# Kernel optimization log

Hardware: AMD Instinct MI355X
Metric: run time of the kernel (lower is better)

## Reference

```python
import jax, jax.numpy as jnp
import numpy as np

EPS = 1e-8  # torch CosineSimilarity default eps


def setup_inputs() -> dict:
    key = jax.random.key(0)
    k1, k2, k3, k4 = jax.random.split(key, 4)
    cur_insts = jax.random.randint(k1, (200, 1024), 0, 50000)          # [S, B] token ids
    W = jax.random.normal(k2, (50000, 300), dtype=jnp.float32)          # embedding table
    train_embs = jax.random.normal(k3, (100000, 300), dtype=jnp.float32)  # pooled train embeddings
    y_train = jax.random.randint(k4, (100000,), 0, 1000)                # train labels
    return {"cur_insts": cur_insts, "W": W, "train_embs": train_embs, "y_train": y_train}


def reference(cur_insts, W, train_embs, y_train):
    # Embed + mean-pool over the sequence axis (dim 0 in the torch code)
    x = W[cur_insts].mean(axis=0)                                   # [B, d]
    # Cosine similarity: x.y / (max(||x||,eps) * max(||y||,eps))
    xn = jnp.maximum(jnp.linalg.norm(x, axis=1, keepdims=True), EPS)        # [B, 1]
    tn = jnp.maximum(jnp.linalg.norm(train_embs, axis=1, keepdims=True), EPS)  # [N, 1]
    sims = (x @ train_embs.T) / (xn * tn.T)                         # [B, N]
    nn_idx = jnp.argmax(sims, axis=1)                               # [B]
    scores = jnp.max(sims, axis=1)                                  # [B]
    y_pred = y_train[nn_idx]                                        # [B]
    return y_pred, scores
```

## Files before the change

### kernel.cpp

```cpp
#include <hip/hip_runtime.h>
#include <hip/hip_bf16.h>
#include <stdint.h>

#define EPS 1e-8f

typedef __attribute__((ext_vector_type(8))) short bf16x8;
typedef __attribute__((ext_vector_type(4))) float f32x4;
typedef unsigned long long u64;
typedef unsigned int u32;

constexpr int SEQ = 200;
constexpr int B_  = 1024;
constexpr int D_  = 300;
constexpr int DP  = 320;
constexpr int NT  = 100000;
constexpr int BM = 256, BN = 128, BK = 64;
constexpr int NSTRIP = 784;
constexpr int NTP = NSTRIP * BN;
constexpr int POOL_BLOCKS = B_;
constexpr int TN2_BLOCKS = NTP / 8;
constexpr int CAND_MAX = 8192;
constexpr int RESCORE_BLOCKS = 2048;
#define MARGIN 2e-3f

__device__ __forceinline__ unsigned short f2bf(float f) {
    u32 b = __float_as_uint(f);
    return (unsigned short)((b + 0x7fffu + ((b >> 16) & 1u)) >> 16);
}
__device__ __forceinline__ u32 simkey(float s) {
    u32 b = __float_as_uint(s);
    return (b & 0x80000000u) ? ~b : (b | 0x80000000u);
}
__device__ __forceinline__ void gload_lds16(const void* g, void* l) {
    __builtin_amdgcn_global_load_lds(
        (const __attribute__((address_space(1))) unsigned int*)g,
        (__attribute__((address_space(3))) unsigned int*)l, 16, 0, 0);
}

__global__ __launch_bounds__(640) void pool_kernel(
    const int* __restrict__ ids, const float* __restrict__ W,
    float* __restrict__ x, unsigned short* __restrict__ xh,
    float* __restrict__ rxn, u32* __restrict__ count)
{
    const int tid = threadIdx.x;
    const int w = tid >> 6, lane = tid & 63;
    const int b = blockIdx.x;
    if (b == 0 && tid == 0) *count = 0;
    __shared__ int sid[SEQ];
    __shared__ float part[10 * 304];
    __shared__ float red[320];
    __shared__ float rns_s;
    for (int s = tid; s < SEQ; s += 640) sid[s] = ids[s * B_ + b];
    __syncthreads();
    float4 a0 = make_float4(0.f, 0.f, 0.f, 0.f);
    float4 a1 = make_float4(0.f, 0.f, 0.f, 0.f);
    for (int s = w; s < SEQ; s += 10) {
        const float4* Wr = (const float4*)(W + (size_t)sid[s] * D_);
        float4 v = Wr[lane];
        a0.x += v.x; a0.y += v.y; a0.z += v.z; a0.w += v.w;
        if (lane < 11) {
            float4 u = Wr[64 + lane];
            a1.x += u.x; a1.y += u.y; a1.z += u.z; a1.w += u.w;
        }
    }
    *(float4*)&part[w * 304 + lane * 4] = a0;
    if (lane < 11) *(float4*)&part[w * 304 + 256 + lane * 4] = a1;
    else if (lane == 11) {
        float4 z = make_float4(0.f, 0.f, 0.f, 0.f);
        *(float4*)&part[w * 304 + 256 + lane * 4] = z;
    }
    __syncthreads();
    float xv = 0.f;
    if (tid < 304) {
        float s = 0.f;
        #pragma unroll
        for (int ww = 0; ww < 10; ++ww) s += part[ww * 304 + tid];
        xv = s * (1.0f / SEQ);
    }
    if (tid < 320) red[tid] = (tid < D_) ? xv * xv : 0.f;
    __syncthreads();
    if (tid < 64) {
        float s = 0.f;
        #pragma unroll
        for (int i = 0; i < 5; ++i) s += red[tid + i * 64];
        #pragma unroll
        for (int m = 32; m >= 1; m >>= 1) s += __shfl_xor(s, m, 64);
        if (tid == 0) {
            float r = 1.0f / fmaxf(sqrtf(s), EPS);
            rxn[b] = r;
            rns_s = r;
        }
    }
    __syncthreads();
    const float rns = rns_s;
    if (tid < 320) {
        if (tid < D_) {
            x[(size_t)b * D_ + tid] = xv;
            xh[(size_t)b * DP + tid] = f2bf(xv * rns);
        } else {
            xh[(size_t)b * DP + tid] = 0;
        }
    }
}

__global__ __launch_bounds__(512) void tnorm_kernel(
    const float* __restrict__ T, unsigned short* __restrict__ Tb)
{
    const int tid = threadIdx.x;
    const int w = tid >> 6, lane = tid & 63;
    const int n = blockIdx.x * 8 + w;
    if (n >= NTP) return;
    ushort4* tb = (ushort4*)(Tb + (size_t)n * DP);
    if (n >= NT) {
        ushort4 z = {0, 0, 0, 0};
        tb[lane] = z;
        if (lane < 16) tb[64 + lane] = z;
        return;
    }
    const float4* Tr = (const float4*)(T + (size_t)n * D_);
    float4 v = Tr[lane];
    float s = v.x * v.x + v.y * v.y + v.z * v.z + v.w * v.w;
    float4 w2 = make_float4(0.f, 0.f, 0.f, 0.f);
    if (lane < 11) {
        w2 = Tr[64 + lane];
        s += w2.x * w2.x + w2.y * w2.y + w2.z * w2.z + w2.w * w2.w;
    }
    #pragma unroll
    for (int m = 32; m >= 1; m >>= 1) s += __shfl_xor(s, m, 64);
    const float rns = 1.0f / fmaxf(sqrtf(s), EPS);
    ushort4 o;
    o.x = f2bf(v.x * rns); o.y = f2bf(v.y * rns);
    o.z = f2bf(v.z * rns); o.w = f2bf(v.w * rns);
    tb[lane] = o;
    if (lane < 16) {
        ushort4 p = {0, 0, 0, 0};
        if (lane < 11) {
            p.x = f2bf(w2.x * rns); p.y = f2bf(w2.y * rns);
            p.z = f2bf(w2.z * rns); p.w = f2bf(w2.w * rns);
        }
        tb[64 + lane] = p;
    }
}

__global__ __launch_bounds__(512, 2) void gemm_hh_kernel(
    const unsigned short* __restrict__ Ah, const unsigned short* __restrict__ Tb,
    float* __restrict__ blockmax)
{
    __shared__ unsigned short sA[BM * BK];
    __shared__ unsigned short sB[BN * BK];
    __shared__ float sBestF[BM * 2];

    const int tid = threadIdx.x;
    const int g = blockIdx.x;
    const int k8 = g & 7;
    const int h = g >> 3;
    const int bMi = h & 3;
    const int strip = ((h >> 2) << 3) | k8;

    const int lane = tid & 63, wid = tid >> 6;
    const int wm = wid >> 1, wn = wid & 1;
    const int quad = lane >> 4, l15 = lane & 15;

    const unsigned short* pA[4];
    int laA[4];
    #pragma unroll
    for (int j = 0; j < 4; ++j) {
        int L = (j * 8 + wid) * 64 + lane;
        int r = L >> 3, c = (L & 7) ^ (r & 7);
        laA[j] = (j * 8 + wid) * 1024;
        pA[j] = Ah + (size_t)(bMi * BM + r) * DP + c * 8;
    }
    const unsigned short* pB[2];
    int laB[2];
    #pragma unroll
    for (int j = 0; j < 2; ++j) {
        int L = (j * 8 + wid) * 64 + lane;
        int r = L >> 3, c = (L & 7) ^ (r & 7);
        laB[j] = (j * 8 + wid) * 1024;
        pB[j] = Tb + (size_t)(strip * BN + r) * DP + c * 8;
    }

    f32x4 acc[4][4] = {};

    for (int kp = 0; kp < DP; kp += BK) {
        #pragma unroll
        for (int j = 0; j < 4; ++j)
            gload_lds16(pA[j] + kp, (char*)sA + laA[j]);
        #pragma unroll
        for (int j = 0; j < 2; ++j)
            gload_lds16(pB[j] + kp, (char*)sB + laB[j]);
        __syncthreads();

        #pragma unroll
        for (int s = 0; s < 2; ++s) {
            bf16x8 fa[4], fb[4];
            #pragma unroll
            for (int f = 0; f < 4; ++f) {
                int ar = wm * 64 + f * 16 + l15;
                int ac = (s * 4 + quad) ^ (ar & 7);
                fa[f] = *(const bf16x8*)&sA[ar * BK + ac * 8];
                int br = wn * 64 + f * 16 + l15;
                int bc = (s * 4 + quad) ^ (br & 7);
                fb[f] = *(const bf16x8*)&sB[br * BK + bc * 8];
            }
            #pragma unroll
            for (int fm = 0; fm < 4; ++fm)
                #pragma unroll
                for (int fn = 0; fn < 4; ++fn)
                    acc[fm][fn] = __builtin_amdgcn_mfma_f32_16x16x32_bf16(
                        fa[fm], fb[fn], acc[fm][fn], 0, 0, 0);
        }
        __syncthreads();
    }

    #pragma unroll
    for (int fm = 0; fm < 4; ++fm) {
        float v[4];
        #pragma unroll
        for (int r = 0; r < 4; ++r) {
            v[r] = fmaxf(fmaxf(acc[fm][0][r], acc[fm][1][r]),
                         fmaxf(acc[fm][2][r], acc[fm][3][r]));
        }
        #pragma unroll
        for (int m = 1; m < 16; m <<= 1) {
            #pragma unroll
            for (int r = 0; r < 4; ++r)
                v[r] = fmaxf(v[r], __shfl_xor(v[r], m, 64));
        }
        if (l15 == 0) {
            int rowbase = wm * 64 + fm * 16 + quad * 4;
            #pragma unroll
            for (int r = 0; r < 4; ++r)
                sBestF[(rowbase + r) * 2 + wn] = v[r];
        }
    }
    __syncthreads();
    if (tid < BM)
        blockmax[(size_t)(bMi * BM + tid) * NSTRIP + strip] =
            fmaxf(sBestF[tid * 2], sBestF[tid * 2 + 1]);
}

__global__ __launch_bounds__(256) void scan_kernel(
    const float* __restrict__ blockmax, u32* __restrict__ cand,
    u32* __restrict__ count, u64* __restrict__ winner)
{
    const int row = blockIdx.x;
    const int t = threadIdx.x;
    const int w = t >> 6, lane = t & 63;
    const float* bmr = blockmax + (size_t)row * NSTRIP;

    __shared__ float wred[4];
    __shared__ float thr_s;
    if (t == 0) winner[row] = 0ull;
    float m = -1e30f;
    for (int j = t; j < NSTRIP; j += 256) m = fmaxf(m, bmr[j]);
    #pragma unroll
    for (int msk = 32; msk >= 1; msk >>= 1) m = fmaxf(m, __shfl_xor(m, msk, 64));
    if (lane == 0) wred[w] = m;
    __syncthreads();
    if (t == 0) {
        float gmx = fmaxf(fmaxf(wred[0], wred[1]), fmaxf(wred[2], wred[3]));
        thr_s = gmx - MARGIN;
    }
    __syncthreads();
    const float thr = thr_s;
    for (int j = t; j < NSTRIP; j += 256) {
        if (bmr[j] >= thr) {
            u32 p = atomicAdd(count, 1u);
            if (p < CAND_MAX) cand[p] = ((u32)row << 10) | (u32)j;
        }
    }
}

__global__ __launch_bounds__(256) void rescore_kernel(
    const u32* __restrict__ cand, const u32* __restrict__ count,
    const float* __restrict__ x, const float* __restrict__ T,
    const float* __restrict__ rxn, u64* __restrict__ winner)
{
    u32 cnt = *count; if (cnt > CAND_MAX) cnt = CAND_MAX;
    __shared__ float4 xs4[75];
    const int t = threadIdx.x;
    const int w = t >> 6, lane = t & 63;
    const int lane4 = lane & 3, colw = lane >> 2;

    for (u32 ci = blockIdx.x; ci < cnt; ci += RESCORE_BLOCKS) {
        const u32 c = cand[ci];
        const int row = c >> 10, strip = c & 1023;
        __syncthreads();
        if (t < 75) xs4[t] = *(const float4*)&x[(size_t)row * D_ + t * 4];
        __syncthreads();
        const float rx = rxn[row];
        u64 best = 0ull;
        #pragma unroll
        for (int p = 0; p < 2; ++p) {
            const int n = strip * BN + w * 32 + p * 16 + colw;
            if (n < NT) {
                const float4* Tr = (const float4*)(T + (size_t)n * D_);
                float dot = 0.f, tt = 0.f;
                #pragma unroll
                for (int jj = 0; jj < 19; ++jj) {
                    int idx = lane4 + jj * 4;
                    if (idx < 75) {
                        float4 v = Tr[idx], xv = xs4[idx];
                        dot += v.x * xv.x + v.y * xv.y + v.z * xv.z + v.w * xv.w;
                        tt  += v.x * v.x + v.y * v.y + v.z * v.z + v.w * v.w;
                    }
                }
                dot += __shfl_xor(dot, 1, 64); tt += __shfl_xor(tt, 1, 64);
                dot += __shfl_xor(dot, 2, 64); tt += __shfl_xor(tt, 2, 64);
                float sim = dot * rx / fmaxf(sqrtf(tt), EPS);
                u64 pk = ((u64)simkey(sim) << 32) | (u32)(~n);
                best = (pk > best) ? pk : best;
            }
        }
        #pragma unroll
        for (int m = 1; m < 64; m <<= 1) {
            u64 o = __shfl_xor(best, m, 64);
            best = (o > best) ? o : best;
        }
        if (lane == 0 && best) atomicMax(&winner[row], best);
    }
}

__global__ __launch_bounds__(64) void final_kernel(
    const u64* __restrict__ winner, const float* __restrict__ x,
    const float* __restrict__ T, const int* __restrict__ y_train,
    float* __restrict__ out)
{
    const int b = blockIdx.x;
    const int lane = threadIdx.x;
    int idx = (int)(~(u32)winner[b]);
    if (idx < 0 || idx >= NT) idx = 0;
    double dot = 0.0, nx = 0.0, nt = 0.0;
    for (int d = lane; d < D_; d += 64) {
        double xv = (double)x[(size_t)b * D_ + d];
        double tv = (double)T[(size_t)idx * D_ + d];
        dot += xv * tv; nx += xv * xv; nt += tv * tv;
    }
    #pragma unroll
    for (int m = 32; m >= 1; m >>= 1) {
        dot += __shfl_xor(dot, m, 64);
        nx  += __shfl_xor(nx, m, 64);
        nt  += __shfl_xor(nt, m, 64);
    }
    if (lane == 0) {
        double score = dot / (fmax(sqrt(nx), (double)EPS) * fmax(sqrt(nt), (double)EPS));
        out[b]      = (float)y_train[idx];
        out[B_ + b] = (float)score;
    }
}

extern "C" void kernel_launch(void* const* d_in, const int* in_sizes, int n_in,
                              void* d_out, int out_size, void* d_ws, size_t ws_size,
                              hipStream_t stream)
{
    const int*   ids = (const int*)d_in[0];
    const float* W   = (const float*)d_in[1];
    const float* T   = (const float*)d_in[2];
    const int*   y   = (const int*)d_in[3];

    char* ws = (char*)d_ws;
    size_t off = 0;
    float* x           = (float*)(ws + off);          off += (size_t)B_ * D_ * 4;
    unsigned short* xh = (unsigned short*)(ws + off); off += (size_t)B_ * DP * 2;
    float* rxn         = (float*)(ws + off);          off += (size_t)B_ * 4;
    unsigned short* Tb = (unsigned short*)(ws + off); off += (size_t)NTP * DP * 2;
    float* blockmax    = (float*)(ws + off);          off += (size_t)B_ * NSTRIP * 4;
    u32* cand          = (u32*)(ws + off);            off += (size_t)CAND_MAX * 4;
    u64* winner        = (u64*)(ws + off);            off += (size_t)B_ * 8;
    u32* count         = (u32*)(ws + off);            off += 256;

    pool_kernel<<<POOL_BLOCKS, 640, 0, stream>>>(ids, W, x, xh, rxn, count);
    tnorm_kernel<<<TN2_BLOCKS, 512, 0, stream>>>(T, Tb);
    gemm_hh_kernel<<<NSTRIP * 4, 512, 0, stream>>>(xh, Tb, blockmax);
    scan_kernel<<<B_, 256, 0, stream>>>(blockmax, cand, count, winner);
    rescore_kernel<<<RESCORE_BLOCKS, 256, 0, stream>>>(cand, count, x, T, rxn, winner);
    final_kernel<<<B_, 64, 0, stream>>>(winner, x, T, y, (float*)d_out);
}
```

Measured before the change: 372.7 us.

## Triple-buffer GEMM K-loop with async global-to-LDS prefetch two steps ahead

Restructures the bf16 similarity GEMM main loop from a single-buffered BK=64 tile with two barriers per step into a three-slot ring of BK=32 tiles. Loads for step t+2 are issued while step t computes, with explicit vmcnt waits and one barrier per step. The LDS swizzle is adapted to the narrower 32-element rows. This is meant to hide global load latency behind the MFMA work, at the cost of more K iterations and a higher barrier count relative to the compute done per step.

Measured after the change: 373.4 us. About the same (+0.2%).

```diff
diff --git a/kernel.cpp b/kernel.cpp
--- a/kernel.cpp
+++ b/kernel.cpp
@@ -14,7 +14,9 @@
 constexpr int D_  = 300;
 constexpr int DP  = 320;
 constexpr int NT  = 100000;
-constexpr int BM = 256, BN = 128, BK = 64;
+constexpr int BM = 256, BN = 128;
+constexpr int BK2 = 32;
+constexpr int KSTEPS = DP / BK2;
 constexpr int NSTRIP = 784;
 constexpr int NTP = NSTRIP * BN;
 constexpr int POOL_BLOCKS = B_;
@@ -146,8 +148,8 @@
     const unsigned short* __restrict__ Ah, const unsigned short* __restrict__ Tb,
     float* __restrict__ blockmax)
 {
-    __shared__ unsigned short sA[BM * BK];
-    __shared__ unsigned short sB[BN * BK];
+    __shared__ unsigned short sA[3][BM * BK2];
+    __shared__ unsigned short sB[3][BN * BK2];
     __shared__ float sBestF[BM * 2];
 
     const int tid = threadIdx.x;
@@ -161,56 +163,63 @@
     const int wm = wid >> 1, wn = wid & 1;
     const int quad = lane >> 4, l15 = lane & 15;
 
-    const unsigned short* pA[4];
-    int laA[4];
-    #pragma unroll
-    for (int j = 0; j < 4; ++j) {
-        int L = (j * 8 + wid) * 64 + lane;
-        int r = L >> 3, c = (L & 7) ^ (r & 7);
-        laA[j] = (j * 8 + wid) * 1024;
+    const unsigned short* pA[2];
+    int laA[2];
+    #pragma unroll
+    for (int j = 0; j < 2; ++j) {
+        int L = j * 512 + tid;
+        int r = L >> 2, c = (L & 3) ^ ((r >> 1) & 3);
+        laA[j] = L * 16;
         pA[j] = Ah + (size_t)(bMi * BM + r) * DP + c * 8;
     }
-    const unsigned short* pB[2];
-    int laB[2];
-    #pragma unroll
-    for (int j = 0; j < 2; ++j) {
-        int L = (j * 8 + wid) * 64 + lane;
-        int r = L >> 3, c = (L & 7) ^ (r & 7);
-        laB[j] = (j * 8 + wid) * 1024;
-        pB[j] = Tb + (size_t)(strip * BN + r) * DP + c * 8;
-    }
+    const unsigned short* pB0;
+    int laB0;
+    {
+        int L = tid;
+        int r = L >> 2, c = (L & 3) ^ ((r >> 1) & 3);
+        laB0 = L * 16;
+        pB0 = Tb + (size_t)(strip * BN + r) * DP + c * 8;
+    }
+
+    auto STAGE = [&](int slot, int kp) {
+        gload_lds16(pA[0] + kp, (char*)sA[slot] + laA[0]);
+        gload_lds16(pA[1] + kp, (char*)sA[slot] + laA[1]);
+        gload_lds16(pB0   + kp, (char*)sB[slot] + laB0);
+    };
 
     f32x4 acc[4][4] = {};
 
-    for (int kp = 0; kp < DP; kp += BK) {
-        #pragma unroll
-        for (int j = 0; j < 4; ++j)
-            gload_lds16(pA[j] + kp, (char*)sA + laA[j]);
-        #pragma unroll
-        for (int j = 0; j < 2; ++j)
-            gload_lds16(pB[j] + kp, (char*)sB + laB[j]);
-        __syncthreads();
-
-        #pragma unroll
-        for (int s = 0; s < 2; ++s) {
-            bf16x8 fa[4], fb[4];
+    STAGE(0, 0);
+    STAGE(1, BK2);
+
+    #pragma unroll
+    for (int t = 0; t < KSTEPS; ++t) {
+        if (t < KSTEPS - 1)
+            asm volatile("s_waitcnt vmcnt(3)" ::: "memory");
+        else
+            asm volatile("s_waitcnt vmcnt(0)" ::: "memory");
+        __builtin_amdgcn_sched_barrier(0);
+        __builtin_amdgcn_s_barrier();
+        __builtin_amdgcn_sched_barrier(0);
+        if (t + 2 < KSTEPS) STAGE((t + 2) % 3, (t + 2) * BK2);
+
+        const int sl = t % 3;
+        bf16x8 fa[4], fb[4];
+        #pragma unroll
+        for (int f = 0; f < 4; ++f) {
+            int ar = wm * 64 + f * 16 + l15;
+            int aq = quad ^ ((ar >> 1) & 3);
+            fa[f] = *(const bf16x8*)&sA[sl][ar * BK2 + aq * 8];
+            int br = wn * 64 + f * 16 + l15;
+            int bq = quad ^ ((br >> 1) & 3);
+            fb[f] = *(const bf16x8*)&sB[sl][br * BK2 + bq * 8];
+        }
+        #pragma unroll
+        for (int fm = 0; fm < 4; ++fm)
             #pragma unroll
-            for (int f = 0; f < 4; ++f) {
-                int ar = wm * 64 + f * 16 + l15;
-                int ac = (s * 4 + quad) ^ (ar & 7);
-                fa[f] = *(const bf16x8*)&sA[ar * BK + ac * 8];
-                int br = wn * 64 + f * 16 + l15;
-                int bc = (s * 4 + quad) ^ (br & 7);
-                fb[f] = *(const bf16x8*)&sB[br * BK + bc * 8];
-            }
-            #pragma unroll
-            for (int fm = 0; fm < 4; ++fm)
-                #pragma unroll
-                for (int fn = 0; fn < 4; ++fn)
-                    acc[fm][fn] = __builtin_amdgcn_mfma_f32_16x16x32_bf16(
-                        fa[fm], fb[fn], acc[fm][fn], 0, 0, 0);
-        }
-        __syncthreads();
+            for (int fn = 0; fn < 4; ++fn)
+                acc[fm][fn] = __builtin_amdgcn_mfma_f32_16x16x32_bf16(
+                    fa[fm], fb[fn], acc[fm][fn], 0, 0, 0);
     }
 
     #pragma unroll
```
